# Kernel tuning notes

Measured on AMD Instinct MI355X. Metric: run time of the kernel, lower is better.

The kernel has to match this reference:

```python
import jax, jax.numpy as jnp
import numpy as np
from functools import partial

EDGES = [(1,2),(1,3),(1,4),(1,5),(1,6),(2,3),(2,7),(2,8),(3,4),(3,9),(4,5),(4,10),(5,6),(5,11),(6,12),(6,13),(7,8),(7,14),(8,9),(8,14),(9,10),(9,15),(10,11),(10,16),(11,12),(11,17),(12,13),(12,18),(13,18),(14,15),(14,19),(15,16),(15,19),(16,17),(16,20),(17,18),(17,21),(18,21),(19,20),(19,22),(20,21),(20,22),(21,22),(24,25),(24,29),(25,26),(25,29),(26,17),(26,30),(27,28),(27,31),(28,31),(29,30),(29,32),(30,31),(30,32),(31,32),(34,35),(34,39),(35,36),(35,39),(36,37),(36,30),(37,18),(37,41),(38,41),(39,40),(39,42),(30,41),(30,42),(31,42),(44,45),(44,49),(45,46),(45,49),(46,47),(46,50),(47,48),(47,51),(48,51),(49,50),(49,52),(50,51),(50,52),(51,52),(54,55),(54,59),(55,56),(55,59),(56,57),(56,60),(57,58),(57,61),(58,61),(59,60),(59,62),(50,61),(60,62),(61,62)]

B, C, T = 32, 64, 4000
F1, D, F2, NCLS = 8, 2, 16, 4
KLEN, GK = 64, 8


def _bn_pack(k, c):
    kg, kb = jax.random.split(k)
    g = jax.random.uniform(kg, (c,), minval=0.5, maxval=1.5)
    b = 0.1 * jax.random.normal(kb, (c,))
    return jnp.stack([g, b, jnp.zeros(c), jnp.ones(c)])  # gamma, beta, mean, var


def setup_inputs() -> dict:
    key = jax.random.key(0)
    ks = jax.random.split(key, 16)
    A = np.zeros((C, C), np.float32)
    for i, j in EDGES:
        A[i - 1, j - 1] = 1.0
        A[j - 1, i - 1] = 1.0
    np.fill_diagonal(A, 1.0)
    feat = F2 * ((T // 4 + 1) // 8)  # 16 * 125 = 2000
    s = 0.1
    return {
        "x": jax.random.normal(ks[0], (B, C, T), jnp.float32),
        "adjacency": jnp.asarray(A),
        "conv1_w": s * jax.random.normal(ks[1], (F1, 1, 1, KLEN), jnp.float32),
        "bnF1": jnp.stack([_bn_pack(jax.random.fold_in(ks[2], i), F1) for i in range(4)]),
        "imp": jax.random.normal(ks[3], (3, F1, C, C), jnp.float32),
        "gconv_w": s * jax.random.normal(ks[4], (3, F1, F1, 1, GK), jnp.float32),
        "dw_w": s * jax.random.normal(ks[5], (F1 * D, 1, C, 1), jnp.float32),
        "bn_sp": _bn_pack(ks[6], F1 * D),
        "sep_dw_w": s * jax.random.normal(ks[7], (F1 * D, 1, 1, 16), jnp.float32),
        "sep_pw_w": s * jax.random.normal(ks[8], (F2, F1 * D, 1, 1), jnp.float32),
        "bn_sep": _bn_pack(ks[9], F2),
        "fc_w": s * jax.random.normal(ks[10], (NCLS, feat), jnp.float32),
        "fc_b": jnp.zeros((NCLS,), jnp.float32),
    }


def _conv(x, w, pad, groups=1):
    return jax.lax.conv_general_dilated(
        x, w, (1, 1), pad, dimension_numbers=("NCHW", "OIHW", "NCHW"),
        feature_group_count=groups)


def _bn(x, p, eps=1e-3):
    g, b, m, v = p
    scale = g * jax.lax.rsqrt(v + eps)
    return x * scale[None, :, None, None] + (b - m * scale)[None, :, None, None]


def reference(x, adjacency, conv1_w, bnF1, imp, gconv_w, dw_w, bn_sp,
              sep_dw_w, sep_pw_w, bn_sep, fc_w, fc_b):
    Bv = x.shape[0]
    h = x[:, None, :, :]                                    # (B,1,C,T)
    h = _conv(h, conv1_w, [(0, 0), (31, 32)])                # 'same' for k=64
    h = _bn(h, bnF1[0])
    for l in range(3):                                       # GraphTemporalConvolution x3
        A = adjacency[None] * imp[l]                         # (F1,C,C) masked importance
        h = jnp.einsum("fcd,bfdt->bfct", A, h)
        h = _conv(h, gconv_w[l], [(0, 0), (3, 4)])           # 'same' for k=8
        h = jax.nn.elu(_bn(h, bnF1[l + 1]))
    # spatial depthwise conv with max-norm constraint (renorm, no grad through scale)
    norms = jnp.sqrt(jnp.sum(dw_w ** 2, axis=(1, 2, 3), keepdims=True))
    scale = jax.lax.stop_gradient(jnp.minimum(1.0, 1.0 / jnp.maximum(norms, 1e-7)))
    h = _conv(h, dw_w * scale, [(0, 0), (0, 0)], groups=F1)  # (B,F1*D,1,T)
    h = jax.nn.elu(_bn(h, bn_sp))
    h = h.reshape(Bv, F1 * D, 1, T // 4, 4).mean(-1)         # AvgPool (1,4)
    # separable conv
    h = _conv(h, sep_dw_w, [(0, 0), (8, 8)], groups=F1 * D)  # width T/4 + 1
    h = _conv(h, sep_pw_w, [(0, 0), (0, 0)])
    h = jax.nn.elu(_bn(h, bn_sep))
    W = h.shape[-1]
    Wp = (W // 8) * 8
    h = h[..., :Wp].reshape(Bv, F2, 1, Wp // 8, 8).mean(-1)  # AvgPool (1,8)
    feat = h.reshape(Bv, -1)
    return feat @ fc_w.T + fc_b
```

## Files before the change

### kernel.cpp

```cpp
#include <hip/hip_runtime.h>


#define B_   32
#define C_   64
#define T_   4000
#define F1_  8
#define TP_  1000
#define W2_  1001
#define MAXDEG 16
#define ROW4 66
#define ROWD 264

typedef _Float16 h16x2 __attribute__((ext_vector_type(2)));
typedef _Float16 f16x8 __attribute__((ext_vector_type(8)));
typedef float    f32x4 __attribute__((ext_vector_type(4)));
typedef __fp16   cvt16x2 __attribute__((ext_vector_type(2)));

static __device__ __forceinline__ float bf2f(unsigned short h) {
  union { unsigned int u; float f; } v; v.u = ((unsigned int)h) << 16; return v.f;
}
static __device__ __forceinline__ unsigned short f2bf(float f) {
  union { float f; unsigned int u; } v; v.f = f;
  unsigned int r = v.u + 0x7FFFu + ((v.u >> 16) & 1u);
  return (unsigned short)(r >> 16);
}
static __device__ __forceinline__ float lo_h(unsigned int u) {
  union { unsigned int u; _Float16 h[2]; } v; v.u = u; return (float)v.h[0];
}
static __device__ __forceinline__ unsigned int pack2h(float a, float b) {
  union { _Float16 h[2]; unsigned int u; } v;
  v.h[0] = (_Float16)a; v.h[1] = (_Float16)b; return v.u;
}
#if defined(__has_builtin) && __has_builtin(__builtin_amdgcn_cvt_pkrtz)
static __device__ __forceinline__ unsigned int pkh(float a, float b) {
  union { cvt16x2 h; unsigned int u; } v;
  v.h = __builtin_amdgcn_cvt_pkrtz(a, b);
  return v.u;
}
#else
static __device__ __forceinline__ unsigned int pkh(float a, float b) {
  return pack2h(a, b);
}
#endif
static __device__ __forceinline__ h16x2 as_h2(unsigned int u) {
  union { unsigned int u; h16x2 h; } v; v.u = u; return v.h;
}
static __device__ __forceinline__ unsigned int alignb(unsigned int hi,
                                                      unsigned int lo,
                                                      unsigned int s) {
  return (unsigned int)(((((unsigned long long)hi) << 32) | lo) >> s);
}
#define PERM_LO(y, x) __builtin_amdgcn_perm((y), (x), 0x05040100u)
#define PERM_HI(y, x) __builtin_amdgcn_perm((y), (x), 0x07060302u)
#if defined(__has_builtin) && __has_builtin(__builtin_amdgcn_fdot2)
#define DOT2(a, b, c) __builtin_amdgcn_fdot2((a), (b), (c), false)
#else
static __device__ __forceinline__ float dot2_fb(h16x2 a, h16x2 b, float c) {
  return fmaf((float)a[0], (float)b[0], fmaf((float)a[1], (float)b[1], c));
}
#define DOT2(a, b, c) dot2_fb((a), (b), (c))
#endif
static __device__ __forceinline__ float eluf(float z) {
  return z > 0.0f ? z : __expf(z) - 1.0f;
}
static __device__ __forceinline__ float ldin(const void* p, int i, int isf32) {
  return isf32 ? ((const float*)p)[i] : bf2f(((const unsigned short*)p)[i]);
}

__global__ __launch_bounds__(256) void k0_setup(
    const void* __restrict__ adj, const void* __restrict__ imp,
    const void* __restrict__ dww, const void* __restrict__ w1,
    const void* __restrict__ bnF, const void* __restrict__ gw,
    const void* __restrict__ bnsp, const void* __restrict__ sdw,
    const void* __restrict__ pw, const void* __restrict__ bnsep,
    const void* __restrict__ fcw, const void* __restrict__ fcb,
    int* __restrict__ flag, int* __restrict__ deg, int* __restrict__ col,
    uint4* __restrict__ w1mf,
    uint4* __restrict__ wmf, float* __restrict__ dwn,
    float* __restrict__ sdwc, float* __restrict__ pwc,
    float* __restrict__ fcwc, float* __restrict__ fcbc,
    float* __restrict__ bnFs, float* __restrict__ bnsps,
    float* __restrict__ bnseps,
    unsigned int* __restrict__ dwph)
{
  __shared__ float dwr[1024];
  __shared__ float dsc[16];
  int tid = threadIdx.x;
  int isf32 = (((const float*)adj)[0] == 1.0f) ? 1 : 0;
  if (tid == 0) *flag = isf32;

  for (int idx = tid; idx < 128; idx += 256) {
    int kk = idx >> 6, l = idx & 63;
    int o = l & 7, q = (l >> 4) & 3;
    uint4 v;
    int bi = o*64 + 32*kk + 8*q;
    v.x = pack2h(ldin(w1, bi+0, isf32), ldin(w1, bi+1, isf32));
    v.y = pack2h(ldin(w1, bi+2, isf32), ldin(w1, bi+3, isf32));
    v.z = pack2h(ldin(w1, bi+4, isf32), ldin(w1, bi+5, isf32));
    v.w = pack2h(ldin(w1, bi+6, isf32), ldin(w1, bi+7, isf32));
    w1mf[idx] = v;
  }
  for (int idx = tid; idx < 384; idx += 256) {
    int lf = idx >> 6;
    int layer = lf >> 1, frag = lf & 1;
    int lane2 = idx & 63;
    int o = lane2 & 7, ii = (lane2 >> 4) + 4*frag;
    uint4 v;
    int bi = layer*512 + (o*8 + ii)*8;
    v.x = pack2h(ldin(gw, bi+0, isf32), ldin(gw, bi+1, isf32));
    v.y = pack2h(ldin(gw, bi+2, isf32), ldin(gw, bi+3, isf32));
    v.z = pack2h(ldin(gw, bi+4, isf32), ldin(gw, bi+5, isf32));
    v.w = pack2h(ldin(gw, bi+6, isf32), ldin(gw, bi+7, isf32));
    wmf[idx] = v;
  }
  for (int i = tid; i < 256;  i += 256) sdwc[i] = ldin(sdw, i, isf32);
  for (int i = tid; i < 256;  i += 256) pwc[i]  = ldin(pw, i, isf32);
  for (int i = tid; i < 8000; i += 256) fcwc[i] = ldin(fcw, i, isf32);
  if (tid < 4) fcbc[tid] = ldin(fcb, tid, isf32);
  for (int i = tid; i < 1024; i += 256) dwr[i] = ldin(dww, i, isf32);

  if (tid < 64) {
    int c = tid, n = 0;
    for (int e = 0; e < MAXDEG; ++e) col[c*MAXDEG + e] = c;
    for (int d = 0; d < 64; ++d) {
      if (ldin(adj, c*64 + d, isf32) != 0.0f) {
        if (n < MAXDEG) col[c*MAXDEG + n] = d;
        ++n;
      }
    }
    deg[c] = n < MAXDEG ? n : MAXDEG;
  }
  __syncthreads();
  if (tid < 16) {
    float s2 = 0.0f;
    for (int c2 = 0; c2 < 64; ++c2) { float wv = dwr[tid*64 + c2]; s2 += wv*wv; }
    dsc[tid] = fminf(1.0f, 1.0f / fmaxf(sqrtf(s2), 1e-7f));
  }
  if (tid >= 64 && tid < 96) {
    int i = tid - 64, s = i >> 3, f = i & 7;
    float g = ldin(bnF, s*32 + f,      isf32);
    float b = ldin(bnF, s*32 + 8 + f,  isf32);
    float m = ldin(bnF, s*32 + 16 + f, isf32);
    float v = ldin(bnF, s*32 + 24 + f, isf32);
    float sc = g * rsqrtf(v + 1e-3f);
    bnFs[s*16 + f] = sc; bnFs[s*16 + 8 + f] = b - m*sc;
  }
  if (tid >= 96 && tid < 112) {
    int ch = tid - 96;
    float g = ldin(bnsp, ch, isf32), b = ldin(bnsp, 16 + ch, isf32);
    float m = ldin(bnsp, 32 + ch, isf32), v = ldin(bnsp, 48 + ch, isf32);
    float sc = g * rsqrtf(v + 1e-3f);
    bnsps[ch] = sc; bnsps[16 + ch] = b - m*sc;
  }
  if (tid >= 112 && tid < 128) {
    int ch = tid - 112;
    float g = ldin(bnsep, ch, isf32), b = ldin(bnsep, 16 + ch, isf32);
    float m = ldin(bnsep, 32 + ch, isf32), v = ldin(bnsep, 48 + ch, isf32);
    float sc = g * rsqrtf(v + 1e-3f);
    bnseps[ch] = sc; bnseps[16 + ch] = b - m*sc;
  }
  __syncthreads();
  for (int i = tid; i < 1024; i += 256) dwn[i] = dwr[i] * dsc[i >> 6];
  __syncthreads();
  for (int idx = tid; idx < 512; idx += 256) {
    int ch = idx >> 5, p = idx & 31;
    dwph[idx] = pack2h(dwr[ch*64 + 2*p]   * dsc[ch],
                       dwr[ch*64 + 2*p+1] * dsc[ch]);
  }
}

__global__ __launch_bounds__(256) void k0b_avals(
    const void* __restrict__ adj, const void* __restrict__ imp,
    const int* __restrict__ flag,
    const int* __restrict__ deg, const int* __restrict__ col,
    float* __restrict__ avals, unsigned int* __restrict__ avph)
{
  int combo = blockIdx.x * 256 + threadIdx.x;
  int isf32 = *flag;
  int c = combo & 63;
  int lf = combo >> 6;
  int dg = deg[c];
  float av[MAXDEG];
  for (int e = 0; e < MAXDEG; ++e) {
    float v = 0.0f;
    if (e < dg) {
      int d = col[c*MAXDEG + e];
      v = ldin(adj, c*64 + d, isf32) * ldin(imp, (lf*64 + c)*64 + d, isf32);
    }
    av[e] = v;
    avals[combo*MAXDEG + e] = v;
  }
  for (int p = 0; p < 8; ++p)
    avph[combo*8 + p] = pack2h(av[2*p], av[2*p + 1]);
}

__global__ __launch_bounds__(256, 4) void k1_conv1_bn(
    const void* __restrict__ x,
    const uint4* __restrict__ w1mf,
    const float* __restrict__ bnFs,
    const int* __restrict__ flag,
    unsigned short* __restrict__ outp)
{
  __shared__ __align__(16) unsigned int xs[548];
  int tid = threadIdx.x;
  int bc = blockIdx.y;
  int b = bc >> 6, c = bc & 63;
  int tb = blockIdx.x * 1024;
  int isf32 = *flag;
  int row = bc * T_;
  if (isf32) {
    const float* xr = (const float*)x + row;
    for (int m = tid; m < 274; m += 256) {
      int tg = tb - 36 + 4*m;
      uint2 st;
      if (tg >= 0 && tg + 3 < T_) {
        float4 v = *(const float4*)(xr + tg);
        st.x = pkh(v.x, v.y); st.y = pkh(v.z, v.w);
      } else {
        float q0 = (tg   >= 0 && tg   < T_) ? xr[tg]   : 0.0f;
        float q1 = (tg+1 >= 0 && tg+1 < T_) ? xr[tg+1] : 0.0f;
        float q2 = (tg+2 >= 0 && tg+2 < T_) ? xr[tg+2] : 0.0f;
        float q3 = (tg+3 >= 0 && tg+3 < T_) ? xr[tg+3] : 0.0f;
        st.x = pkh(q0, q1); st.y = pkh(q2, q3);
      }
      *(uint2*)(xs + 2*m) = st;
    }
  } else {
    const unsigned short* xr = (const unsigned short*)x + row;
    for (int m = tid; m < 274; m += 256) {
      int tg = tb - 36 + 4*m;
      uint2 st;
      if (tg >= 0 && tg + 3 < T_) {
        uint2 v = *(const uint2*)(xr + tg);
        st.x = pkh(bf2f((unsigned short)(v.x & 0xFFFFu)),
                   bf2f((unsigned short)(v.x >> 16)));
        st.y = pkh(bf2f((unsigned short)(v.y & 0xFFFFu)),
                   bf2f((unsigned short)(v.y >> 16)));
      } else {
        float q0 = (tg   >= 0 && tg   < T_) ? bf2f(xr[tg])   : 0.0f;
        float q1 = (tg+1 >= 0 && tg+1 < T_) ? bf2f(xr[tg+1]) : 0.0f;
        float q2 = (tg+2 >= 0 && tg+2 < T_) ? bf2f(xr[tg+2]) : 0.0f;
        float q3 = (tg+3 >= 0 && tg+3 < T_) ? bf2f(xr[tg+3]) : 0.0f;
        st.x = pkh(q0, q1); st.y = pkh(q2, q3);
      }
      *(uint2*)(xs + 2*m) = st;
    }
  }
  __syncthreads();

  int lane = tid & 63;
  int wv4 = tid >> 6;
  int m = lane & 15, q = lane >> 4;
  int sel = (m >> 3) & 1;
  union { uint4 u; f16x8 h; } w0u, w1u;
  w0u.u = w1mf[lane];
  w1u.u = w1mf[64 + lane];
  int o8 = m & 7;
  float sc  = bnFs[o8];
  float shb = bnFs[8 + o8];
  const unsigned int* p0 = xs + 2 + m + 4*q + 128*wv4;
  unsigned short* orow = outp + (size_t)((b*8 + o8)*64 + c) * T_;
  #pragma unroll
  for (int s = 0; s < 8; ++s) {
    unsigned dwa[5], dwb[5];
    #pragma unroll
    for (int j = 0; j < 5; ++j) {
      dwa[j] = p0[16*s + j];
      dwb[j] = p0[16*s + 16 + j];
    }
    union { unsigned d[4]; f16x8 h; } Ae0, Ao0, Ae1, Ao1;
    #pragma unroll
    for (int j = 0; j < 4; ++j) {
      Ao0.d[j] = dwa[j+1];
      Ae0.d[j] = alignb(dwa[j+1], dwa[j], 16);
      Ao1.d[j] = dwb[j+1];
      Ae1.d[j] = alignb(dwb[j+1], dwb[j], 16);
    }
    f32x4 ae = {0.0f, 0.0f, 0.0f, 0.0f};
    f32x4 ao = {0.0f, 0.0f, 0.0f, 0.0f};
    ae = __builtin_amdgcn_mfma_f32_16x16x32_f16(Ae0.h, w0u.h, ae, 0, 0, 0);
    ae = __builtin_amdgcn_mfma_f32_16x16x32_f16(Ae1.h, w1u.h, ae, 0, 0, 0);
    ao = __builtin_amdgcn_mfma_f32_16x16x32_f16(Ao0.h, w0u.h, ao, 0, 0, 0);
    ao = __builtin_amdgcn_mfma_f32_16x16x32_f16(Ao1.h, w1u.h, ao, 0, 0, 0);
    float y0 = sel ? ae[2] : ae[0];
    float y1 = sel ? ao[2] : ao[0];
    float y2 = sel ? ae[3] : ae[1];
    float y3 = sel ? ao[3] : ao[1];
    int t0g = tb + wv4*256 + s*32 + 8*q + 4*sel;
    if (t0g < T_) {
      uint2 st;
      st.x = pkh(y0*sc + shb, y1*sc + shb);
      st.y = pkh(y2*sc + shb, y3*sc + shb);
      *(uint2*)(orow + t0g) = st;
    }
  }
}

__global__ __launch_bounds__(256, 8) void k23_gcn_gconv(
    const unsigned short* __restrict__ in,
    unsigned short* __restrict__ outp,
    const int* __restrict__ deg, const int* __restrict__ col,
    const float* __restrict__ avals,
    const unsigned int* __restrict__ avph,
    const uint4* __restrict__ wmf,
    const float* __restrict__ bnFs, int l)
{
  __shared__ __align__(16) uint4 ash[8 * ROW4];
  int tid = threadIdx.x;
  int wgid = blockIdx.y * 8 + blockIdx.x;
  int swz  = (wgid & 7) * 2048 + (wgid >> 3);
  int c = swz & 63;
  int xt = (swz >> 6) & 7;
  int b = swz >> 9;
  int tb = xt * 512;
  int wb = tb - 8;
  int dg = deg[c];
  const int* cp = col + c*MAXDEG;

  {
    int i = tid >> 5;
    int mlane = tid & 31;
    int dgp = (dg + 1) >> 1;
    const unsigned int* wpp = avph + ((l*8 + i)*64 + c) * 8;
    const float* av = avals + ((l*8 + i)*64 + c) * MAXDEG;
    const unsigned short* rbp = in + (size_t)((b*8 + i) * 64) * T_;
    for (int m = mlane; m < ROW4; m += 32) {
      int t = wb + 8*m;
      float a[8] = {0,0,0,0,0,0,0,0};
      if (t >= 0 && t + 7 < T_) {
        for (int p = 0; p < dgp; ++p) {
          int d0 = cp[2*p];
          int d1 = cp[2*p + 1];
          h16x2 w2 = as_h2(wpp[p]);
          uint4 v0 = *(const uint4*)(rbp + d0*T_ + t);
          uint4 v1 = *(const uint4*)(rbp + d1*T_ + t);
          a[0] = DOT2(as_h2(PERM_LO(v1.x, v0.x)), w2, a[0]);
          a[1] = DOT2(as_h2(PERM_HI(v1.x, v0.x)), w2, a[1]);
          a[2] = DOT2(as_h2(PERM_LO(v1.y, v0.y)), w2, a[2]);
          a[3] = DOT2(as_h2(PERM_HI(v1.y, v0.y)), w2, a[3]);
          a[4] = DOT2(as_h2(PERM_LO(v1.z, v0.z)), w2, a[4]);
          a[5] = DOT2(as_h2(PERM_HI(v1.z, v0.z)), w2, a[5]);
          a[6] = DOT2(as_h2(PERM_LO(v1.w, v0.w)), w2, a[6]);
          a[7] = DOT2(as_h2(PERM_HI(v1.w, v0.w)), w2, a[7]);
        }
      } else if (t + 7 >= 0 && t < T_) {
        for (int e = 0; e < dg; ++e) {
          int d = cp[e];
          float wv = av[e];
          const unsigned short* rp = rbp + d*T_;
          #pragma unroll
          for (int q = 0; q < 8; ++q) {
            int tq = t + q;
            if (tq >= 0 && tq < T_)
              a[q] = fmaf(wv, lo_h((unsigned int)rp[tq]), a[q]);
          }
        }
      }
      uint4 o;
      o.x = pkh(a[0], a[1]); o.y = pkh(a[2], a[3]);
      o.z = pkh(a[4], a[5]); o.w = pkh(a[6], a[7]);
      ash[i*ROW4 + m] = o;
    }
  }
  __syncthreads();

  int lane = tid & 63;
  int wv4 = tid >> 6;
  int m = lane & 15, q = lane >> 4;
  int sel = (m >> 3) & 1;
  union { uint4 u; f16x8 h; } w0u, w1u;
  w0u.u = wmf[(l*2 + 0)*64 + lane];
  w1u.u = wmf[(l*2 + 1)*64 + lane];
  int o8 = m & 7;
  float sc  = bnFs[(l+1)*16 + o8];
  float shb = bnFs[(l+1)*16 + 8 + o8];
  const unsigned int* ashd = (const unsigned int*)ash;
  const unsigned int* p0 = ashd + q*ROWD + wv4*64 + m + 2;
  const unsigned int* p1 = p0 + 4*ROWD;
  unsigned short* orow = outp + (size_t)((b*8 + o8)*64 + c) * T_;
  #pragma unroll
  for (int s = 0; s < 4; ++s) {
    unsigned dwa[5], dwb[5];
    #pragma unroll
    for (int j = 0; j < 5; ++j) {
      dwa[j] = p0[16*s + j];
      dwb[j] = p1[16*s + j];
    }
    union { unsigned d[4]; f16x8 h; } Ae0, Ao0, Ae1, Ao1;
    #pragma unroll
    for (int j = 0; j < 4; ++j) {
      Ao0.d[j] = dwa[j+1];
      Ae0.d[j] = alignb(dwa[j+1], dwa[j], 16);
      Ao1.d[j] = dwb[j+1];
      Ae1.d[j] = alignb(dwb[j+1], dwb[j], 16);
    }
    f32x4 ae = {0.0f, 0.0f, 0.0f, 0.0f};
    f32x4 ao = {0.0f, 0.0f, 0.0f, 0.0f};
    ae = __builtin_amdgcn_mfma_f32_16x16x32_f16(Ae0.h, w0u.h, ae, 0, 0, 0);
    ae = __builtin_amdgcn_mfma_f32_16x16x32_f16(Ae1.h, w1u.h, ae, 0, 0, 0);
    ao = __builtin_amdgcn_mfma_f32_16x16x32_f16(Ao0.h, w0u.h, ao, 0, 0, 0);
    ao = __builtin_amdgcn_mfma_f32_16x16x32_f16(Ao1.h, w1u.h, ao, 0, 0, 0);
    float y0 = sel ? ae[2] : ae[0];
    float y1 = sel ? ao[2] : ao[0];
    float y2 = sel ? ae[3] : ae[1];
    float y3 = sel ? ao[3] : ao[1];
    int t0g = tb + wv4*128 + s*32 + 8*q + 4*sel;
    if (t0g < T_) {
      uint2 st;
      st.x = pkh(eluf(y0*sc + shb), eluf(y1*sc + shb));
      st.y = pkh(eluf(y2*sc + shb), eluf(y3*sc + shb));
      *(uint2*)(orow + t0g) = st;
    }
  }
}

__global__ __launch_bounds__(256) void k4_dw(
    const unsigned short* __restrict__ in,
    const unsigned int* __restrict__ dwph,
    const float* __restrict__ bnsps,
    float* __restrict__ p1)
{
  int tid = threadIdx.x;
  int bg = blockIdx.y;
  int b = bg >> 3, g = bg & 7;
  int tile = blockIdx.x * 256 + tid;
  if (tile >= 500) return;
  int t0 = tile * 8;
  int base = bg * (64 * T_);
  const unsigned int* w0pp = dwph + (2*g)*32;
  const unsigned int* w1pp = dwph + (2*g + 1)*32;
  float a0[8] = {0,0,0,0,0,0,0,0}, a1[8] = {0,0,0,0,0,0,0,0};
  for (int p = 0; p < 32; ++p) {
    h16x2 w02 = as_h2(w0pp[p]);
    h16x2 w12 = as_h2(w1pp[p]);
    uint4 v0 = *(const uint4*)(in + base + (2*p)*T_ + t0);
    uint4 v1 = *(const uint4*)(in + base + (2*p + 1)*T_ + t0);
    unsigned pr;
    pr = PERM_LO(v1.x, v0.x);
    a0[0] = DOT2(as_h2(pr), w02, a0[0]); a1[0] = DOT2(as_h2(pr), w12, a1[0]);
    pr = PERM_HI(v1.x, v0.x);
    a0[1] = DOT2(as_h2(pr), w02, a0[1]); a1[1] = DOT2(as_h2(pr), w12, a1[1]);
    pr = PERM_LO(v1.y, v0.y);
    a0[2] = DOT2(as_h2(pr), w02, a0[2]); a1[2] = DOT2(as_h2(pr), w12, a1[2]);
    pr = PERM_HI(v1.y, v0.y);
    a0[3] = DOT2(as_h2(pr), w02, a0[3]); a1[3] = DOT2(as_h2(pr), w12, a1[3]);
    pr = PERM_LO(v1.z, v0.z);
    a0[4] = DOT2(as_h2(pr), w02, a0[4]); a1[4] = DOT2(as_h2(pr), w12, a1[4]);
    pr = PERM_HI(v1.z, v0.z);
    a0[5] = DOT2(as_h2(pr), w02, a0[5]); a1[5] = DOT2(as_h2(pr), w12, a1[5]);
    pr = PERM_LO(v1.w, v0.w);
    a0[6] = DOT2(as_h2(pr), w02, a0[6]); a1[6] = DOT2(as_h2(pr), w12, a1[6]);
    pr = PERM_HI(v1.w, v0.w);
    a0[7] = DOT2(as_h2(pr), w02, a0[7]); a1[7] = DOT2(as_h2(pr), w12, a1[7]);
  }
  float sc0 = bnsps[2*g],     sh0 = bnsps[16 + 2*g];
  float sc1 = bnsps[2*g + 1], sh1 = bnsps[16 + 2*g + 1];
  int oi = t0 >> 2;
  float2 r0, r1;
  r0.x = 0.25f * (eluf(a0[0]*sc0+sh0) + eluf(a0[1]*sc0+sh0)
                + eluf(a0[2]*sc0+sh0) + eluf(a0[3]*sc0+sh0));
  r0.y = 0.25f * (eluf(a0[4]*sc0+sh0) + eluf(a0[5]*sc0+sh0)
                + eluf(a0[6]*sc0+sh0) + eluf(a0[7]*sc0+sh0));
  r1.x = 0.25f * (eluf(a1[0]*sc1+sh1) + eluf(a1[1]*sc1+sh1)
                + eluf(a1[2]*sc1+sh1) + eluf(a1[3]*sc1+sh1));
  r1.y = 0.25f * (eluf(a1[4]*sc1+sh1) + eluf(a1[5]*sc1+sh1)
                + eluf(a1[6]*sc1+sh1) + eluf(a1[7]*sc1+sh1));
  *(float2*)(p1 + (b*16 + 2*g)*TP_ + oi)     = r0;
  *(float2*)(p1 + (b*16 + 2*g + 1)*TP_ + oi) = r1;
}

__global__ __launch_bounds__(256) void k5_sep(
    const float* __restrict__ p1,
    const float* __restrict__ sdwc,
    const float* __restrict__ pwc,
    const float* __restrict__ bnseps,
    float* __restrict__ p2)
{
  __shared__ float ps[16*272];
  int tid = threadIdx.x;
  int wq = blockIdx.x, b = blockIdx.y;
  int wb = wq * 256;
  for (int ch = 0; ch < 16; ++ch) {
    for (int s = tid; s < 272; s += 256) {
      int t = wb - 8 + s;
      ps[ch*272 + s] = (t >= 0 && t < TP_) ? p1[(b*16 + ch)*TP_ + t] : 0.0f;
    }
  }
  __syncthreads();
  int w0 = wb + tid;
  if (w0 >= W2_) return;
  float dws[16];
  for (int ch = 0; ch < 16; ++ch) {
    float a = 0.0f;
    #pragma unroll
    for (int k = 0; k < 16; ++k)
      a = fmaf(sdwc[ch*16 + k], ps[ch*272 + tid + k], a);
    dws[ch] = a;
  }
  for (int f = 0; f < 16; ++f) {
    float a = 0.0f;
    #pragma unroll
    for (int ch = 0; ch < 16; ++ch) a = fmaf(pwc[f*16 + ch], dws[ch], a);
    float sc = bnseps[f], sh = bnseps[16 + f];
    p2[(b*16 + f)*W2_ + w0] = eluf(a*sc + sh);
  }
}

__global__ __launch_bounds__(256) void k6_fc(
    const float* __restrict__ p2,
    const float* __restrict__ fcwc,
    const float* __restrict__ fcbc,
    const int* __restrict__ flag,
    void* __restrict__ outp)
{
  __shared__ float red[4*256];
  int tid = threadIdx.x;
  int b = blockIdx.x;
  float part[4] = {0.0f, 0.0f, 0.0f, 0.0f};
  for (int idx = tid; idx < 2000; idx += 256) {
    int f = idx / 125, q = idx - f*125;
    const float* src = p2 + (b*16 + f)*W2_ + q*8;
    float s = src[0]+src[1]+src[2]+src[3]+src[4]+src[5]+src[6]+src[7];
    float mval = 0.125f * s;
    #pragma unroll
    for (int n = 0; n < 4; ++n) part[n] = fmaf(fcwc[n*2000 + idx], mval, part[n]);
  }
  #pragma unroll
  for (int n = 0; n < 4; ++n) red[n*256 + tid] = part[n];
  __syncthreads();
  for (int s = 128; s > 0; s >>= 1) {
    if (tid < s) {
      #pragma unroll
      for (int n = 0; n < 4; ++n) red[n*256 + tid] += red[n*256 + tid + s];
    }
    __syncthreads();
  }
  if (tid < 4) {
    float val = red[tid*256] + fcbc[tid];
    if (*flag) ((float*)outp)[b*4 + tid] = val;
    else       ((unsigned short*)outp)[b*4 + tid] = f2bf(val);
  }
}

extern "C" void kernel_launch(void* const* d_in, const int* in_sizes, int n_in,
                              void* d_out, int out_size, void* d_ws, size_t ws_size,
                              hipStream_t stream) {
  const void* x     = d_in[0];
  const void* adj   = d_in[1];
  const void* w1    = d_in[2];
  const void* bnF   = d_in[3];
  const void* imp   = d_in[4];
  const void* gw    = d_in[5];
  const void* dww   = d_in[6];
  const void* bnsp  = d_in[7];
  const void* sdw   = d_in[8];
  const void* pw    = d_in[9];
  const void* bnsep = d_in[10];
  const void* fcw   = d_in[11];
  const void* fcb   = d_in[12];

  char* w = (char*)d_ws;
  const size_t OFF = 262144000;
  unsigned short* bufA = (unsigned short*)(w);
  unsigned short* bufB = (unsigned short*)(w + 131072000);
  int*   flag   = (int*)  (w + OFF + 0);
  int*   deg    = (int*)  (w + OFF + 256);
  int*   col    = (int*)  (w + OFF + 512);
  float* avals  = (float*)(w + OFF + 4608);
  float* dwn    = (float*)(w + OFF + 108032);
  float* sdwc   = (float*)(w + OFF + 112128);
  float* pwc    = (float*)(w + OFF + 113152);
  float* fcwc   = (float*)(w + OFF + 114176);
  float* fcbc   = (float*)(w + OFF + 146176);
  float* bnFs   = (float*)(w + OFF + 146432);
  float* bnsps  = (float*)(w + OFF + 146688);
  float* bnseps = (float*)(w + OFF + 146944);
  float* p1     = (float*)(w + OFF + 147200);
  float* p2     = (float*)(w + OFF + 2195200);
  uint4* wmf    = (uint4*)(w + OFF + 4245248);
  unsigned int* avph = (unsigned int*)(w + OFF + 4251392);
  unsigned int* dwph = (unsigned int*)(w + OFF + 4300544);
  uint4* w1mf   = (uint4*)(w + OFF + 4302592);

  k0_setup<<<1, 256, 0, stream>>>(adj, imp, dww, w1, bnF, gw, bnsp, sdw, pw,
                                  bnsep, fcw, fcb, flag, deg, col,
                                  w1mf, wmf, dwn, sdwc, pwc, fcwc, fcbc,
                                  bnFs, bnsps, bnseps, dwph);
  k0b_avals<<<6, 256, 0, stream>>>(adj, imp, flag, deg, col, avals, avph);
  k1_conv1_bn<<<dim3(4, B_*C_), 256, 0, stream>>>(x, w1mf, bnFs, flag, bufA);
  for (int l = 0; l < 3; ++l) {
    const unsigned short* src = (l & 1) ? bufB : bufA;
    unsigned short*       dst = (l & 1) ? bufA : bufB;
    k23_gcn_gconv<<<dim3(8, B_*C_), 256, 0, stream>>>(src, dst, deg, col,
                                                      avals, avph, wmf, bnFs, l);
  }
  k4_dw<<<dim3(2, B_*F1_), 256, 0, stream>>>(bufB, dwph, bnsps, p1);
  k5_sep<<<dim3(4, B_), 256, 0, stream>>>(p1, sdwc, pwc, bnseps, p2);
  k6_fc<<<32, 256, 0, stream>>>(p2, fcwc, fcbc, flag, d_out);
}
```

Measured before the change: 467.7 us.

## Double GCN time tile to 1024 and fuse separable conv with FC via atomics

The graph-conv kernel now handles 1024 time steps per block instead of 512. This halves the grid and amortises the 8-sample halo and the neighbour-gather setup over more outputs, at the cost of larger shared memory and lower occupancy (launch bounds 6). The separable-conv kernel also computes the avg-pool and FC partial sums directly and adds them into a small accumulator with atomics. This removes the p2 buffer round trip and the separate FC reduction kernel, and a tiny kernel now applies the bias and writes the output.

After: 452.5 us. 1.03x faster.

```diff
diff --git a/kernel.cpp b/kernel.cpp
--- a/kernel.cpp
+++ b/kernel.cpp
@@ -8,8 +8,8 @@
 #define TP_  1000
 #define W2_  1001
 #define MAXDEG 16
-#define ROW4 66
-#define ROWD 264
+#define ROW4 130
+#define ROWD 520
 
 typedef _Float16 h16x2 __attribute__((ext_vector_type(2)));
 typedef _Float16 f16x8 __attribute__((ext_vector_type(8)));
@@ -81,13 +81,15 @@
     float* __restrict__ fcwc, float* __restrict__ fcbc,
     float* __restrict__ bnFs, float* __restrict__ bnsps,
     float* __restrict__ bnseps,
-    unsigned int* __restrict__ dwph)
+    unsigned int* __restrict__ dwph,
+    float* __restrict__ fcacc)
 {
   __shared__ float dwr[1024];
   __shared__ float dsc[16];
   int tid = threadIdx.x;
   int isf32 = (((const float*)adj)[0] == 1.0f) ? 1 : 0;
   if (tid == 0) *flag = isf32;
+  if (tid < 128) fcacc[tid] = 0.0f;
 
   for (int idx = tid; idx < 128; idx += 256) {
     int kk = idx >> 6, l = idx & 63;
@@ -296,7 +298,7 @@
   }
 }
 
-__global__ __launch_bounds__(256, 8) void k23_gcn_gconv(
+__global__ __launch_bounds__(256, 6) void k23_gcn_gconv(
     const unsigned short* __restrict__ in,
     unsigned short* __restrict__ outp,
     const int* __restrict__ deg, const int* __restrict__ col,
@@ -307,12 +309,12 @@
 {
   __shared__ __align__(16) uint4 ash[8 * ROW4];
   int tid = threadIdx.x;
-  int wgid = blockIdx.y * 8 + blockIdx.x;
-  int swz  = (wgid & 7) * 2048 + (wgid >> 3);
+  int wgid = blockIdx.y * 4 + blockIdx.x;
+  int swz  = (wgid & 7) * 1024 + (wgid >> 3);
   int c = swz & 63;
-  int xt = (swz >> 6) & 7;
-  int b = swz >> 9;
-  int tb = xt * 512;
+  int xt = (swz >> 6) & 3;
+  int b = swz >> 8;
+  int tb = xt * 1024;
   int wb = tb - 8;
   int dg = deg[c];
   const int* cp = col + c*MAXDEG;
@@ -375,11 +377,11 @@
   float sc  = bnFs[(l+1)*16 + o8];
   float shb = bnFs[(l+1)*16 + 8 + o8];
   const unsigned int* ashd = (const unsigned int*)ash;
-  const unsigned int* p0 = ashd + q*ROWD + wv4*64 + m + 2;
+  const unsigned int* p0 = ashd + q*ROWD + wv4*128 + m + 2;
   const unsigned int* p1 = p0 + 4*ROWD;
   unsigned short* orow = outp + (size_t)((b*8 + o8)*64 + c) * T_;
   #pragma unroll
-  for (int s = 0; s < 4; ++s) {
+  for (int s = 0; s < 8; ++s) {
     unsigned dwa[5], dwb[5];
     #pragma unroll
     for (int j = 0; j < 5; ++j) {
@@ -404,7 +406,7 @@
     float y1 = sel ? ao[2] : ao[0];
     float y2 = sel ? ae[3] : ae[1];
     float y3 = sel ? ao[3] : ao[1];
-    int t0g = tb + wv4*128 + s*32 + 8*q + 4*sel;
+    int t0g = tb + wv4*256 + s*32 + 8*q + 4*sel;
     if (t0g < T_) {
       uint2 st;
       st.x = pkh(eluf(y0*sc + shb), eluf(y1*sc + shb));
@@ -469,14 +471,17 @@
   *(float2*)(p1 + (b*16 + 2*g + 1)*TP_ + oi) = r1;
 }
 
-__global__ __launch_bounds__(256) void k5_sep(
+__global__ __launch_bounds__(256) void k5_sep_fc(
     const float* __restrict__ p1,
     const float* __restrict__ sdwc,
     const float* __restrict__ pwc,
     const float* __restrict__ bnseps,
-    float* __restrict__ p2)
+    const float* __restrict__ fcwc,
+    float* __restrict__ fcacc)
 {
   __shared__ float ps[16*272];
+  __shared__ float vals[16*256];
+  __shared__ float red[4*64];
   int tid = threadIdx.x;
   int wq = blockIdx.x, b = blockIdx.y;
   int wb = wq * 256;
@@ -488,7 +493,7 @@
   }
   __syncthreads();
   int w0 = wb + tid;
-  if (w0 >= W2_) return;
+  bool valid = (w0 < TP_);
   float dws[16];
   for (int ch = 0; ch < 16; ++ch) {
     float a = 0.0f;
@@ -502,44 +507,47 @@
     #pragma unroll
     for (int ch = 0; ch < 16; ++ch) a = fmaf(pwc[f*16 + ch], dws[ch], a);
     float sc = bnseps[f], sh = bnseps[16 + f];
-    p2[(b*16 + f)*W2_ + w0] = eluf(a*sc + sh);
-  }
-}
-
-__global__ __launch_bounds__(256) void k6_fc(
-    const float* __restrict__ p2,
-    const float* __restrict__ fcwc,
-    const float* __restrict__ fcbc,
-    const int* __restrict__ flag,
-    void* __restrict__ outp)
+    vals[f*256 + tid] = valid ? eluf(a*sc + sh) : 0.0f;
+  }
+  __syncthreads();
+  float part[4] = {0.0f, 0.0f, 0.0f, 0.0f};
+  #pragma unroll
+  for (int it = 0; it < 2; ++it) {
+    int item = it*256 + tid;
+    int ch = item >> 5, g = item & 31;
+    int j = wq*32 + g;
+    if (j < 125) {
+      const float* vp = vals + ch*256 + 8*g;
+      float s8 = vp[0]+vp[1]+vp[2]+vp[3]+vp[4]+vp[5]+vp[6]+vp[7];
+      float mval = 0.125f * s8;
+      int fi = ch*125 + j;
+      #pragma unroll
+      for (int n = 0; n < 4; ++n)
+        part[n] = fmaf(fcwc[n*2000 + fi], mval, part[n]);
+    }
+  }
+  #pragma unroll
+  for (int n = 0; n < 4; ++n) {
+    float v = part[n];
+    for (int off = 32; off > 0; off >>= 1) v += __shfl_down(v, off, 64);
+    if ((tid & 63) == 0) red[n*64 + (tid >> 6)] = v;
+  }
+  __syncthreads();
+  if (tid < 4) {
+    float v = red[tid*64 + 0] + red[tid*64 + 1]
+            + red[tid*64 + 2] + red[tid*64 + 3];
+    atomicAdd(&fcacc[b*4 + tid], v);
+  }
+}
+
+__global__ __launch_bounds__(128) void k6c_out(
+    const float* __restrict__ fcacc, const float* __restrict__ fcbc,
+    const int* __restrict__ flag, void* __restrict__ outp)
 {
-  __shared__ float red[4*256];
   int tid = threadIdx.x;
-  int b = blockIdx.x;
-  float part[4] = {0.0f, 0.0f, 0.0f, 0.0f};
-  for (int idx = tid; idx < 2000; idx += 256) {
-    int f = idx / 125, q = idx - f*125;
-    const float* src = p2 + (b*16 + f)*W2_ + q*8;
-    float s = src[0]+src[1]+src[2]+src[3]+src[4]+src[5]+src[6]+src[7];
-    float mval = 0.125f * s;
-    #pragma unroll
-    for (int n = 0; n < 4; ++n) part[n] = fmaf(fcwc[n*2000 + idx], mval, part[n]);
-  }
-  #pragma unroll
-  for (int n = 0; n < 4; ++n) red[n*256 + tid] = part[n];
-  __syncthreads();
-  for (int s = 128; s > 0; s >>= 1) {
-    if (tid < s) {
-      #pragma unroll
-      for (int n = 0; n < 4; ++n) red[n*256 + tid] += red[n*256 + tid + s];
-    }
-    __syncthreads();
-  }
-  if (tid < 4) {
-    float val = red[tid*256] + fcbc[tid];
-    if (*flag) ((float*)outp)[b*4 + tid] = val;
-    else       ((unsigned short*)outp)[b*4 + tid] = f2bf(val);
-  }
+  float val = fcacc[tid] + fcbc[tid & 3];
+  if (*flag) ((float*)outp)[tid] = val;
+  else       ((unsigned short*)outp)[tid] = f2bf(val);
 }
 
 extern "C" void kernel_launch(void* const* d_in, const int* in_sizes, int n_in,
@@ -576,25 +584,26 @@
   float* bnsps  = (float*)(w + OFF + 146688);
   float* bnseps = (float*)(w + OFF + 146944);
   float* p1     = (float*)(w + OFF + 147200);
-  float* p2     = (float*)(w + OFF + 2195200);
   uint4* wmf    = (uint4*)(w + OFF + 4245248);
   unsigned int* avph = (unsigned int*)(w + OFF + 4251392);
   unsigned int* dwph = (unsigned int*)(w + OFF + 4300544);
   uint4* w1mf   = (uint4*)(w + OFF + 4302592);
+  float* fcacc  = (float*)(w + OFF + 4304640);
 
   k0_setup<<<1, 256, 0, stream>>>(adj, imp, dww, w1, bnF, gw, bnsp, sdw, pw,
                                   bnsep, fcw, fcb, flag, deg, col,
                                   w1mf, wmf, dwn, sdwc, pwc, fcwc, fcbc,
-                                  bnFs, bnsps, bnseps, dwph);
+                                  bnFs, bnsps, bnseps, dwph, fcacc);
   k0b_avals<<<6, 256, 0, stream>>>(adj, imp, flag, deg, col, avals, avph);
   k1_conv1_bn<<<dim3(4, B_*C_), 256, 0, stream>>>(x, w1mf, bnFs, flag, bufA);
   for (int l = 0; l < 3; ++l) {
     const unsigned short* src = (l & 1) ? bufB : bufA;
     unsigned short*       dst = (l & 1) ? bufA : bufB;
-    k23_gcn_gconv<<<dim3(8, B_*C_), 256, 0, stream>>>(src, dst, deg, col,
+    k23_gcn_gconv<<<dim3(4, B_*C_), 256, 0, stream>>>(src, dst, deg, col,
                                                       avals, avph, wmf, bnFs, l);
   }
   k4_dw<<<dim3(2, B_*F1_), 256, 0, stream>>>(bufB, dwph, bnsps, p1);
-  k5_sep<<<dim3(4, B_), 256, 0, stream>>>(p1, sdwc, pwc, bnseps, p2);
-  k6_fc<<<32, 256, 0, stream>>>(p2, fcwc, fcbc, flag, d_out);
-}
+  k5_sep_fc<<<dim3(4, B_), 256, 0, stream>>>(p1, sdwc, pwc, bnseps,
+                                             fcwc, fcacc);
+  k6c_out<<<1, 128, 0, stream>>>(fcacc, fcbc, flag, d_out);
+}
```
